# Kernel tuning notes

Hardware: AMD Instinct MI355X
Metric: run time of the kernel (lower is better)

Reference implementation:

```python
import jax, jax.numpy as jnp
import numpy as np

N, E, IN_FEATS, HID, HEADS = 50000, 800000, 256, 32, 8
NEG_SLOPE = 0.2


def _init_params(key):
    ks = jax.random.split(key, 12)
    def lin(k, fi, fo):
        return jax.random.normal(k, (fi, fo), jnp.float32) * (1.0 / np.sqrt(fi))
    p = {}
    # layer 0: in_feats -> HID x HEADS
    p['W0'] = lin(ks[0], IN_FEATS, HEADS * HID)
    p['al0'] = jax.random.normal(ks[1], (HEADS, HID), jnp.float32) * 0.1
    p['ar0'] = jax.random.normal(ks[2], (HEADS, HID), jnp.float32) * 0.1
    p['b0'] = jnp.zeros((HEADS * HID,), jnp.float32)
    # layer 1: HID*HEADS -> HID x HEADS
    p['W1'] = lin(ks[3], HEADS * HID, HEADS * HID)
    p['al1'] = jax.random.normal(ks[4], (HEADS, HID), jnp.float32) * 0.1
    p['ar1'] = jax.random.normal(ks[5], (HEADS, HID), jnp.float32) * 0.1
    p['b1'] = jnp.zeros((HEADS * HID,), jnp.float32)
    # layer 2 (final): HID*HEADS -> HID x 1 head, no activation
    p['W2'] = lin(ks[6], HEADS * HID, HID)
    p['al2'] = jax.random.normal(ks[7], (1, HID), jnp.float32) * 0.1
    p['ar2'] = jax.random.normal(ks[8], (1, HID), jnp.float32) * 0.1
    p['b2'] = jnp.zeros((HID,), jnp.float32)
    return p


def setup_inputs() -> dict:
    key = jax.random.key(0)
    k1, k2, k3, kp = jax.random.split(key, 4)
    inp = {
        'features': jax.random.normal(k1, (N, IN_FEATS), jnp.float32),
        'src': jax.random.randint(k2, (E,), 0, N, jnp.int32),
        'dst': jax.random.randint(k3, (E,), 0, N, jnp.int32),
    }
    inp.update(_init_params(kp))
    return inp


def _gat_layer(x, src, dst, W, al, ar, b, heads, act):
    n = x.shape[0]
    d = W.shape[1] // heads
    feat = (x @ W).reshape(n, heads, d)           # [N,H,D]
    el = jnp.sum(feat * al, axis=-1)              # [N,H]
    er = jnp.sum(feat * ar, axis=-1)              # [N,H]
    e = jax.nn.leaky_relu(el[src] + er[dst], NEG_SLOPE)   # [E,H]
    # segment softmax over destination neighborhoods
    emax = jax.ops.segment_max(e, dst, num_segments=n)
    ex = jnp.exp(e - emax[dst])
    denom = jax.ops.segment_sum(ex, dst, num_segments=n)
    a = ex / (denom[dst] + 1e-9)                  # [E,H]
    msg = feat[src] * a[:, :, None]               # [E,H,D]
    out = jax.ops.segment_sum(msg, dst, num_segments=n)   # [N,H,D]
    out = out + b.reshape(1, heads, d)
    return act(out) if act is not None else out


def reference(features, src, dst, W0, al0, ar0, b0, W1, al1, ar1, b1, W2, al2, ar2, b2):
    h = _gat_layer(features, src, dst, W0, al0, ar0, b0, HEADS, jax.nn.elu)
    h = h.reshape(h.shape[0], -1)
    h = _gat_layer(h, src, dst, W1, al1, ar1, b1, HEADS, jax.nn.elu)
    h = h.reshape(h.shape[0], -1)
    h = _gat_layer(h, src, dst, W2, al2, ar2, b2, 1, None)   # [N,1,D]
    return h.mean(axis=1)                                    # [N,D]
```

## Files before the change

kernel.cpp:

```cpp
#include <hip/hip_runtime.h>

typedef unsigned short u16;
typedef unsigned int   u32;
typedef __attribute__((ext_vector_type(8))) short  short8;
typedef __attribute__((ext_vector_type(4))) float  f32x4;
typedef __attribute__((ext_vector_type(2))) float  f32x2;
typedef __attribute__((ext_vector_type(2))) unsigned int u32v2;
typedef __attribute__((ext_vector_type(4))) unsigned int u32v4;

#define NN 50000
#define NE 800000

__device__ __forceinline__ float bf2f(u16 b) { return __uint_as_float(((u32)b) << 16); }
__device__ __forceinline__ float bflo(u32 p) { return __uint_as_float(p << 16); }
__device__ __forceinline__ float bfhi(u32 p) { return __uint_as_float(p & 0xffff0000u); }
__device__ __forceinline__ u16 f2bf(float f) {
    u32 u = __float_as_uint(f);
    u32 r = u + 0x7fffu + ((u >> 16) & 1u);
    return (u16)(r >> 16);
}
__device__ __forceinline__ float lexp(float v) {
    v = fmaxf(v, 0.2f * v);
    return __expf(fminf(v, 60.f));
}

struct DetectArgs { const u32* p[13]; int nw[13]; };

__global__ __launch_bounds__(256) void k_detect(DetectArgs a, int* flags) {
    __shared__ int sh[256], sz[256];
    int j = blockIdx.x;
    const u32* x = a.p[j];
    int n = a.nw[j];
    int t = threadIdx.x;
    int hits = 0, nz = 0;
    for (int i = t; i < n; i += 256) {
        u32 w = x[i];
        if (w) {
            ++nz;
            u32 e = (w >> 7) & 0xffu;
            if (e >= 100 && e <= 150) ++hits;
        }
    }
    sh[t] = hits; sz[t] = nz;
    __syncthreads();
    for (int ofs = 128; ofs > 0; ofs >>= 1) {
        if (t < ofs) { sh[t] += sh[t + ofs]; sz[t] += sz[t + ofs]; }
        __syncthreads();
    }
    if (t == 0) flags[j] = (sz[0] == 0) ? 2 : ((sh[0] * 2 >= sz[0]) ? 0 : 1);
}

struct ConvArgs { const void* s[9]; float* d[9]; int n[9]; int fi[9]; };

__global__ void k_convert(ConvArgs a, const int* __restrict__ flags) {
    int j = blockIdx.y;
    int i = blockIdx.x * 256 + threadIdx.x;
    if (i >= a.n[j]) return;
    int fl = flags[a.fi[j]];
    float v = 0.f;
    if (fl == 1) v = ((const float*)a.s[j])[i];
    else if (fl == 0) v = bf2f(((const u16*)a.s[j])[i]);
    a.d[j][i] = v;
}

__global__ void k_wpack(const void* __restrict__ Wsrc, const int* __restrict__ flags,
                        int fidx, int N, u16* __restrict__ Wp, int nchunks) {
    int id = blockIdx.x * 256 + threadIdx.x;
    if (id >= nchunks) return;
    int L = id & 63, kt = (id >> 6) & 7, nt = id >> 9;
    int col = nt * 16 + (L & 15);
    int krow = kt * 32 + ((L >> 4) & 3) * 8;
    bool isf32 = (flags[fidx] == 1);
#pragma unroll
    for (int j = 0; j < 8; ++j) {
        int s = (krow + j) * N + col;
        Wp[id * 8 + j] = isf32 ? f2bf(((const float*)Wsrc)[s]) : ((const u16*)Wsrc)[s];
    }
}

__global__ void k_hist(const int* __restrict__ dst, int* __restrict__ deg, int E) {
    int e = blockIdx.x * 256 + threadIdx.x;
    if (e < E) atomicAdd(&deg[dst[e]], 1);
}

__global__ __launch_bounds__(256) void k_scan_partial(const int* __restrict__ deg,
                                                      int* __restrict__ bsum, int n) {
    __shared__ int red[256];
    int t = threadIdx.x;
    int i = blockIdx.x * 256 + t;
    red[t] = (i < n) ? deg[i] : 0;
    __syncthreads();
    for (int ofs = 128; ofs > 0; ofs >>= 1) {
        if (t < ofs) red[t] += red[t + ofs];
        __syncthreads();
    }
    if (t == 0) bsum[blockIdx.x] = red[0];
}

__global__ __launch_bounds__(256) void k_scan_bsum(int* __restrict__ bsum, int nb) {
    __shared__ int s[256];
    int t = threadIdx.x;
    int v = (t < nb) ? bsum[t] : 0;
    s[t] = v;
    __syncthreads();
    for (int ofs = 1; ofs < 256; ofs <<= 1) {
        int x = (t >= ofs) ? s[t - ofs] : 0;
        __syncthreads();
        s[t] += x;
        __syncthreads();
    }
    if (t < nb) bsum[t] = s[t] - v;
}

__global__ __launch_bounds__(256) void k_scan_final(const int* __restrict__ deg,
                                                    const int* __restrict__ bsum,
                                                    int* __restrict__ rowptr,
                                                    int* __restrict__ cursor, int n) {
    __shared__ int s[256];
    int t = threadIdx.x;
    int i = blockIdx.x * 256 + t;
    int v = (i < n) ? deg[i] : 0;
    s[t] = v;
    __syncthreads();
    for (int ofs = 1; ofs < 256; ofs <<= 1) {
        int x = (t >= ofs) ? s[t - ofs] : 0;
        __syncthreads();
        s[t] += x;
        __syncthreads();
    }
    int excl = bsum[blockIdx.x] + s[t] - v;
    if (i < n) {
        rowptr[i] = excl;
        cursor[i] = excl;
        if (i == n - 1) rowptr[n] = excl + v;
    }
}

__global__ void k_scatter(const int* __restrict__ src, const int* __restrict__ dst,
                          int* __restrict__ cursor, int* __restrict__ csr_src, int E) {
    int e = blockIdx.x * 256 + threadIdx.x;
    if (e >= E) return;
    int p = atomicAdd(&cursor[dst[e]], 1);
    csr_src[p] = src[e];
}

__global__ __launch_bounds__(256) void k_gemm_mfma(const void* __restrict__ Xv,
                                                   const int* __restrict__ xflag,
                                                   const u16* __restrict__ Wp,
                                                   u16* __restrict__ OUT, int nrows) {
    __shared__ u16 As[64 * 256];
    const int t = threadIdx.x;
    const int w = t >> 6, L = t & 63;
    const int quad = (L >> 4) & 3;
    const int r0 = blockIdx.x * 64;
    const int nb = blockIdx.y * 8;
    const bool xf32 = (xflag != nullptr) && (*xflag == 1);

    short8* Asv = (short8*)As;
    short8 zero = {0, 0, 0, 0, 0, 0, 0, 0};
#pragma unroll
    for (int i = 0; i < 8; ++i) {
        int g = i * 256 + t;
        int row = g >> 5, cc = g & 31;
        int r = r0 + row;
        short8 val = zero;
        if (r < nrows) {
            if (xf32) {
                const f32x4* Xf4 = (const f32x4*)Xv;
                f32x4 lo = Xf4[(size_t)r * 64 + cc * 2];
                f32x4 hi = Xf4[(size_t)r * 64 + cc * 2 + 1];
                val[0] = (short)f2bf(lo[0]); val[1] = (short)f2bf(lo[1]);
                val[2] = (short)f2bf(lo[2]); val[3] = (short)f2bf(lo[3]);
                val[4] = (short)f2bf(hi[0]); val[5] = (short)f2bf(hi[1]);
                val[6] = (short)f2bf(hi[2]); val[7] = (short)f2bf(hi[3]);
            } else {
                val = ((const short8*)Xv)[(size_t)r * 32 + cc];
            }
        }
        Asv[cc * 64 + (row ^ (cc & 7))] = val;
    }

    const short8* Wv = (const short8*)Wp;
    short8 bf[2][8];
#pragma unroll
    for (int jn = 0; jn < 2; ++jn) {
        int nt = nb + w + jn * 4;
#pragma unroll
        for (int kt = 0; kt < 8; ++kt) bf[jn][kt] = Wv[(nt * 8 + kt) * 64 + L];
    }
    __syncthreads();

    f32x4 acc[4][2];
#pragma unroll
    for (int mi = 0; mi < 4; ++mi)
#pragma unroll
        for (int jn = 0; jn < 2; ++jn) acc[mi][jn] = (f32x4){0.f, 0.f, 0.f, 0.f};

#pragma unroll
    for (int kt = 0; kt < 8; ++kt) {
        const int ccr = kt * 4 + quad;
#pragma unroll
        for (int mi = 0; mi < 4; ++mi) {
            short8 af = Asv[ccr * 64 + ((mi * 16 + (L & 15)) ^ (ccr & 7))];
            acc[mi][0] = __builtin_amdgcn_mfma_f32_16x16x32_bf16(af, bf[0][kt], acc[mi][0], 0, 0, 0);
            acc[mi][1] = __builtin_amdgcn_mfma_f32_16x16x32_bf16(af, bf[1][kt], acc[mi][1], 0, 0, 0);
        }
    }

    const int colbase = blockIdx.y * 128;
#pragma unroll
    for (int mi = 0; mi < 4; ++mi) {
        int rb = r0 + mi * 16 + quad * 4;
#pragma unroll
        for (int jn = 0; jn < 2; ++jn) {
            int c = colbase + (w + jn * 4) * 16 + (L & 15);
            const size_t hb = (size_t)(c >> 5) * nrows * 32 + (c & 31);
#pragma unroll
            for (int reg = 0; reg < 4; ++reg) {
                int r = rb + reg;
                if (r < nrows) OUT[hb + (size_t)r * 32] = f2bf(acc[mi][jn][reg]);
            }
        }
    }
}

__global__ __launch_bounds__(256) void k_gemm_mfma32(const u16* __restrict__ Xb,
                                                     const u16* __restrict__ Wp,
                                                     u16* __restrict__ OUT, int nrows) {
    __shared__ u16 As[128 * 256];
    const int t = threadIdx.x;
    const int w = t >> 6, L = t & 63;
    const int quad = (L >> 4) & 3;
    const int r0 = blockIdx.x * 128;
    const int mh = (w >> 1) * 64, nt = w & 1;

    const short8* Xv = (const short8*)Xb;
    short8* Asv = (short8*)As;
    short8 zero = {0, 0, 0, 0, 0, 0, 0, 0};
#pragma unroll
    for (int i = 0; i < 16; ++i) {
        int g = i * 256 + t;
        int row = g >> 5, cc = g & 31;
        int r = r0 + row;
        Asv[cc * 128 + (row ^ (cc & 7))] = (r < nrows) ? Xv[(size_t)r * 32 + cc] : zero;
    }

    const short8* Wv = (const short8*)Wp;
    short8 bf[8];
#pragma unroll
    for (int kt = 0; kt < 8; ++kt) bf[kt] = Wv[(nt * 8 + kt) * 64 + L];
    __syncthreads();

    f32x4 acc[4];
#pragma unroll
    for (int mi = 0; mi < 4; ++mi) acc[mi] = (f32x4){0.f, 0.f, 0.f, 0.f};

#pragma unroll
    for (int kt = 0; kt < 8; ++kt) {
        const int ccr = kt * 4 + quad;
#pragma unroll
        for (int mi = 0; mi < 4; ++mi) {
            short8 af = Asv[ccr * 128 + ((mh + mi * 16 + (L & 15)) ^ (ccr & 7))];
            acc[mi] = __builtin_amdgcn_mfma_f32_16x16x32_bf16(af, bf[kt], acc[mi], 0, 0, 0);
        }
    }

#pragma unroll
    for (int mi = 0; mi < 4; ++mi) {
        int rb = r0 + mh + mi * 16 + quad * 4;
        int c = nt * 16 + (L & 15);
#pragma unroll
        for (int reg = 0; reg < 4; ++reg) {
            int r = rb + reg;
            if (r < nrows) OUT[(size_t)r * 32 + c] = f2bf(acc[mi][reg]);
        }
    }
}

__global__ void k_elr8(const u16* __restrict__ featT, const float* __restrict__ al,
                       const float* __restrict__ ar, float* __restrict__ elT,
                       float* __restrict__ erT, int n) {
    int node = blockIdx.x * 256 + threadIdx.x;
    int h = blockIdx.y;
    if (node >= n) return;
    const u32v4* fu = (const u32v4*)((const u32*)featT + ((size_t)h * n + node) * 16);
    const float* A = al + h * 32;
    const float* B = ar + h * 32;
    float sl = 0.f, sr = 0.f;
#pragma unroll
    for (int j = 0; j < 4; ++j) {
        u32v4 w4 = fu[j];
#pragma unroll
        for (int k = 0; k < 4; ++k) {
            u32 w = (k == 0) ? w4.x : (k == 1) ? w4.y : (k == 2) ? w4.z : w4.w;
            float f0 = bflo(w), f1 = bfhi(w);
            int c = j * 8 + k * 2;
            sl += f0 * A[c] + f1 * A[c + 1];
            sr += f0 * B[c] + f1 * B[c + 1];
        }
    }
    elT[(size_t)h * n + node] = sl;
    erT[(size_t)h * n + node] = sr;
}

__global__ void k_elr1(const u16* __restrict__ featb, const float* __restrict__ al,
                       const float* __restrict__ ar, float* __restrict__ el,
                       float* __restrict__ er, int n) {
    int node = blockIdx.x * 256 + threadIdx.x;
    if (node >= n) return;
    const u32v4* fu = (const u32v4*)((const u32*)featb + (size_t)node * 16);
    float sl = 0.f, sr = 0.f;
#pragma unroll
    for (int j = 0; j < 4; ++j) {
        u32v4 w4 = fu[j];
#pragma unroll
        for (int k = 0; k < 4; ++k) {
            u32 w = (k == 0) ? w4.x : (k == 1) ? w4.y : (k == 2) ? w4.z : w4.w;
            float f0 = bflo(w), f1 = bfhi(w);
            int c = j * 8 + k * 2;
            sl += f0 * al[c] + f1 * al[c + 1];
            sr += f0 * ar[c] + f1 * ar[c + 1];
        }
    }
    el[node] = sl;
    er[node] = sr;
}

__global__ __launch_bounds__(256) void k_gather8(const int* __restrict__ rowptr,
                                                 const int* __restrict__ csr_src,
                                                 const float* __restrict__ elT,
                                                 const float* __restrict__ erT,
                                                 const u32* __restrict__ featT2,
                                                 const float* __restrict__ bias,
                                                 u32* __restrict__ xout2) {
    const int t = threadIdx.x;
    const int h = blockIdx.x & 7;
    const int g = blockIdx.x >> 3;
    const int d = g * 16 + (t >> 4);
    const int lane = t & 15;
    const int b = rowptr[d], e = rowptr[d + 1];
    const float* __restrict__ elh = elT + (size_t)h * NN;
    const u32* __restrict__ fT = featT2 + (size_t)h * NN * 16;
    const float erd = erT[(size_t)h * NN + d];
    float a0 = 0.f, a1 = 0.f, ssum = 0.f;

    for (int c = b; c < e; c += 16) {
        const int idx = c + lane;
        const int s_own = __builtin_nontemporal_load(csr_src + (idx < e ? idx : e - 1));
        const float ex_own = (idx < e) ? lexp(elh[s_own] + erd) : 0.f;
        ssum += ex_own;
#pragma unroll
        for (int i = 0; i < 16; ++i) {
            const int si = __shfl(s_own, i, 16);
            const float ai = __shfl(ex_own, i, 16);
            const u32 w = fT[(size_t)si * 16 + lane];
            a0 += bflo(w) * ai;
            a1 += bfhi(w) * ai;
        }
    }

    ssum += __shfl_xor(ssum, 1);
    ssum += __shfl_xor(ssum, 2);
    ssum += __shfl_xor(ssum, 4);
    ssum += __shfl_xor(ssum, 8);

    const float rd = 1.f / (ssum + 1e-9f);
    const f32x2 bb = *(const f32x2*)&bias[h * 32 + lane * 2];
    float v0 = a0 * rd + bb[0];
    float v1 = a1 * rd + bb[1];
    v0 = v0 > 0.f ? v0 : expm1f(v0);
    v1 = v1 > 0.f ? v1 : expm1f(v1);
    const u32 o = (u32)f2bf(v0) | ((u32)f2bf(v1) << 16);
    __builtin_nontemporal_store(o, xout2 + ((size_t)d * 128 + h * 16 + lane));
}

__global__ __launch_bounds__(256) void k_gather1(const int* __restrict__ rowptr,
                                                 const int* __restrict__ csr_src,
                                                 const float* __restrict__ el,
                                                 const float* __restrict__ er,
                                                 const u32* __restrict__ featb2,
                                                 const float* __restrict__ bias,
                                                 void* __restrict__ out,
                                                 const int* __restrict__ flag, int n) {
    int t = threadIdx.x;
    int d = blockIdx.x * 16 + (t >> 4);
    int q = t & 15;
    if (d >= n) return;
    int b = rowptr[d], e = rowptr[d + 1];
    float erd = er[d];
    float a0 = 0.f, a1 = 0.f, ssum = 0.f;
    int p = b;
    for (; p + 4 <= e; p += 4) {
        int s0 = csr_src[p], s1 = csr_src[p + 1], s2 = csr_src[p + 2], s3 = csr_src[p + 3];
        float e0 = lexp(el[s0] + erd);
        float e1 = lexp(el[s1] + erd);
        float e2 = lexp(el[s2] + erd);
        float e3 = lexp(el[s3] + erd);
        u32 w0 = featb2[(size_t)s0 * 16 + q];
        u32 w1 = featb2[(size_t)s1 * 16 + q];
        u32 w2 = featb2[(size_t)s2 * 16 + q];
        u32 w3 = featb2[(size_t)s3 * 16 + q];
        a0 += bflo(w0) * e0; a1 += bfhi(w0) * e0;
        a0 += bflo(w1) * e1; a1 += bfhi(w1) * e1;
        a0 += bflo(w2) * e2; a1 += bfhi(w2) * e2;
        a0 += bflo(w3) * e3; a1 += bfhi(w3) * e3;
        ssum += (e0 + e1) + (e2 + e3);
    }
    for (; p < e; ++p) {
        int s = csr_src[p];
        float ev = lexp(el[s] + erd);
        u32 w = featb2[(size_t)s * 16 + q];
        a0 += bflo(w) * ev;
        a1 += bfhi(w) * ev;
        ssum += ev;
    }
    float rd = 1.f / (ssum + 1e-9f);
    float v0 = a0 * rd + bias[2 * q];
    float v1 = a1 * rd + bias[2 * q + 1];
    if (*flag == 1) {
        f32x2 o = {v0, v1};
        ((f32x2*)out)[(size_t)d * 16 + q] = o;
    } else {
        ((u32*)out)[(size_t)d * 16 + q] = (u32)f2bf(v0) | ((u32)f2bf(v1) << 16);
    }
}

extern "C" void kernel_launch(void* const* d_in, const int* in_sizes, int n_in,
                              void* d_out, int out_size, void* d_ws, size_t ws_size,
                              hipStream_t stream) {
    const void* features = d_in[0];
    const int* src = (const int*)d_in[1];
    const int* dst = (const int*)d_in[2];

    char* ws = (char*)d_ws;
    size_t off = 0;
    auto carve = [&](size_t bytes) -> void* {
        void* p = ws + off;
        off = (off + bytes + 255) & ~(size_t)255;
        return p;
    };
    int*   flags = (int*)carve(64);
    float* pconv = (float*)carve(2048 * 4);
    u16*   Wp0 = (u16*)carve(65536 * 2);
    u16*   Wp1 = (u16*)carve(65536 * 2);
    u16*   Wp2 = (u16*)carve(8192 * 2);
    u16*   Xb    = (u16*)carve((size_t)NN * 256 * 2);
    u16*   featb = (u16*)carve((size_t)NN * 256 * 2);
    float* el   = (float*)carve((size_t)NN * 8 * 4);
    float* er   = (float*)carve((size_t)NN * 8 * 4);
    int*   deg     = (int*)carve((size_t)NN * 4);
    int*   cursor  = (int*)carve((size_t)NN * 4);
    int*   rowptr  = (int*)carve((size_t)(NN + 1) * 4);
    int*   bsum    = (int*)carve(256 * 4);
    int*   csr_src = (int*)carve((size_t)NE * 4);
    if (off > ws_size) return;

    const int N = NN, E = NE;
    const int nscan = (N + 255) / 256;

    DetectArgs da;
    const int din_idx[13] = {0, 3, 4, 5, 6, 7, 8, 9, 10, 11, 12, 13, 14};
    for (int j = 0; j < 13; ++j) {
        da.p[j] = (const u32*)d_in[din_idx[j]];
        int nw = in_sizes[din_idx[j]] / 2;
        da.nw[j] = nw > 512 ? 512 : nw;
    }
    k_detect<<<13, 256, 0, stream>>>(da, flags);

    ConvArgs ca;
    const int psl[9] = {4, 5, 6, 8, 9, 10, 12, 13, 14};
    const int pfl[9] = {2, 3, 4, 6, 7, 8, 10, 11, 12};
    float* dsts[9];
    {
        size_t o = 0;
        for (int j = 0; j < 9; ++j) {
            dsts[j] = pconv + o;
            o += (size_t)in_sizes[psl[j]];
        }
    }
    for (int j = 0; j < 9; ++j) {
        ca.s[j] = d_in[psl[j]];
        ca.d[j] = dsts[j];
        ca.n[j] = in_sizes[psl[j]];
        ca.fi[j] = pfl[j];
    }
    k_convert<<<dim3(1, 9), 256, 0, stream>>>(ca, flags);
    float* al0f = dsts[0]; float* ar0f = dsts[1]; float* b0f = dsts[2];
    float* al1f = dsts[3]; float* ar1f = dsts[4]; float* b1f = dsts[5];
    float* al2f = dsts[6]; float* ar2f = dsts[7]; float* b2f = dsts[8];

    k_wpack<<<32, 256, 0, stream>>>(d_in[3],  flags, 1, 256, Wp0, 8192);
    k_wpack<<<32, 256, 0, stream>>>(d_in[7],  flags, 5, 256, Wp1, 8192);
    k_wpack<<<4,  256, 0, stream>>>(d_in[11], flags, 9, 32,  Wp2, 1024);

    hipMemsetAsync(deg, 0, (size_t)N * 4, stream);
    k_hist<<<(E + 255) / 256, 256, 0, stream>>>(dst, deg, E);
    k_scan_partial<<<nscan, 256, 0, stream>>>(deg, bsum, N);
    k_scan_bsum<<<1, 256, 0, stream>>>(bsum, nscan);
    k_scan_final<<<nscan, 256, 0, stream>>>(deg, bsum, rowptr, cursor, N);
    k_scatter<<<(E + 255) / 256, 256, 0, stream>>>(src, dst, cursor, csr_src, E);

    const dim3 ggrid((N + 63) / 64, 2);
    const dim3 egrid(nscan, 8);
    const int ggrid8 = 8 * (N / 16);

    k_gemm_mfma<<<ggrid, 256, 0, stream>>>(features, flags, Wp0, featb, N);
    k_elr8<<<egrid, 256, 0, stream>>>(featb, al0f, ar0f, el, er, N);
    k_gather8<<<ggrid8, 256, 0, stream>>>(rowptr, csr_src, el, er,
                                          (const u32*)featb, b0f, (u32*)Xb);

    k_gemm_mfma<<<ggrid, 256, 0, stream>>>(Xb, nullptr, Wp1, featb, N);
    k_elr8<<<egrid, 256, 0, stream>>>(featb, al1f, ar1f, el, er, N);
    k_gather8<<<ggrid8, 256, 0, stream>>>(rowptr, csr_src, el, er,
                                          (const u32*)featb, b1f, (u32*)Xb);

    k_gemm_mfma32<<<(N + 127) / 128, 256, 0, stream>>>(Xb, Wp2, featb, N);
    k_elr1<<<(N + 255) / 256, 256, 0, stream>>>(featb, al2f, ar2f, el, er, N);
    k_gather1<<<(N + 15) / 16, 256, 0, stream>>>(rowptr, csr_src, el, er,
                                                 (const u32*)featb, b2f,
                                                 d_out, flags, N);
}
```

Baseline: 490.1 us.

## Map one wavefront per destination node in per-head gather with LDS edge staging

The per-head gather kernel now assigns a full 64-lane wavefront to each destination node instead of 16 lanes. Each lane loads 8 bytes, and 8 edges are processed in parallel per iteration. Source indices and exp weights are staged through shared memory rather than broadcast by shuffles. Partial sums are reduced across lane groups at the end. The aim is more memory-level parallelism and wider loads on irregular neighbor rows, at the cost of four times as many blocks, extra cross-lane reductions, and idle lanes for low-degree nodes.

```diff
diff --git a/kernel.cpp b/kernel.cpp
--- a/kernel.cpp
+++ b/kernel.cpp
@@ -333,45 +333,68 @@
                                                  const u32* __restrict__ featT2,
                                                  const float* __restrict__ bias,
                                                  u32* __restrict__ xout2) {
+    __shared__ u32v2 sbuf[4][64];
     const int t = threadIdx.x;
+    const int wv = t >> 6;
+    const int lane = t & 63;
     const int h = blockIdx.x & 7;
-    const int g = blockIdx.x >> 3;
-    const int d = g * 16 + (t >> 4);
-    const int lane = t & 15;
+    const int d = (blockIdx.x >> 3) * 4 + wv;
+    const int j8 = lane >> 3, c8 = lane & 7;
     const int b = rowptr[d], e = rowptr[d + 1];
+    const int deg = e - b;
     const float* __restrict__ elh = elT + (size_t)h * NN;
-    const u32* __restrict__ fT = featT2 + (size_t)h * NN * 16;
+    const u32v2* __restrict__ fv = (const u32v2*)(featT2 + (size_t)h * NN * 16);
     const float erd = erT[(size_t)h * NN + d];
-    float a0 = 0.f, a1 = 0.f, ssum = 0.f;
-
-    for (int c = b; c < e; c += 16) {
-        const int idx = c + lane;
-        const int s_own = __builtin_nontemporal_load(csr_src + (idx < e ? idx : e - 1));
-        const float ex_own = (idx < e) ? lexp(elh[s_own] + erd) : 0.f;
+    u32v2* __restrict__ sb = sbuf[wv];
+
+    float a0 = 0.f, a1 = 0.f, a2 = 0.f, a3 = 0.f, ssum = 0.f;
+
+    for (int c = 0; c < deg; c += 64) {
+        const int nv = deg - c < 64 ? deg - c : 64;
+        const int idx = b + c + (lane < nv ? lane : nv - 1);
+        const int s_own = __builtin_nontemporal_load(csr_src + idx);
+        const float ex_own = (lane < nv) ? lexp(elh[s_own] + erd) : 0.f;
         ssum += ex_own;
-#pragma unroll
-        for (int i = 0; i < 16; ++i) {
-            const int si = __shfl(s_own, i, 16);
-            const float ai = __shfl(ex_own, i, 16);
-            const u32 w = fT[(size_t)si * 16 + lane];
-            a0 += bflo(w) * ai;
-            a1 += bfhi(w) * ai;
-        }
-    }
-
-    ssum += __shfl_xor(ssum, 1);
-    ssum += __shfl_xor(ssum, 2);
-    ssum += __shfl_xor(ssum, 4);
-    ssum += __shfl_xor(ssum, 8);
-
-    const float rd = 1.f / (ssum + 1e-9f);
-    const f32x2 bb = *(const f32x2*)&bias[h * 32 + lane * 2];
-    float v0 = a0 * rd + bb[0];
-    float v1 = a1 * rd + bb[1];
-    v0 = v0 > 0.f ? v0 : expm1f(v0);
-    v1 = v1 > 0.f ? v1 : expm1f(v1);
-    const u32 o = (u32)f2bf(v0) | ((u32)f2bf(v1) << 16);
-    __builtin_nontemporal_store(o, xout2 + ((size_t)d * 128 + h * 16 + lane));
+        u32v2 pr;
+        pr.x = (u32)s_own;
+        pr.y = __float_as_uint(ex_own);
+        sb[lane] = pr;
+        __builtin_amdgcn_sched_barrier(0);
+        const int ni = (nv + 7) >> 3;
+        for (int i = 0; i < ni; ++i) {
+            const u32v2 pr2 = sb[i * 8 + j8];
+            const float ai = __uint_as_float(pr2.y);
+            const u32v2 w = fv[(size_t)pr2.x * 8 + c8];
+            a0 += bflo(w.x) * ai; a1 += bfhi(w.x) * ai;
+            a2 += bflo(w.y) * ai; a3 += bfhi(w.y) * ai;
+        }
+        __builtin_amdgcn_sched_barrier(0);
+    }
+
+    a0 += __shfl_xor(a0, 8); a0 += __shfl_xor(a0, 16); a0 += __shfl_xor(a0, 32);
+    a1 += __shfl_xor(a1, 8); a1 += __shfl_xor(a1, 16); a1 += __shfl_xor(a1, 32);
+    a2 += __shfl_xor(a2, 8); a2 += __shfl_xor(a2, 16); a2 += __shfl_xor(a2, 32);
+    a3 += __shfl_xor(a3, 8); a3 += __shfl_xor(a3, 16); a3 += __shfl_xor(a3, 32);
+    ssum += __shfl_xor(ssum, 1);  ssum += __shfl_xor(ssum, 2);
+    ssum += __shfl_xor(ssum, 4);  ssum += __shfl_xor(ssum, 8);
+    ssum += __shfl_xor(ssum, 16); ssum += __shfl_xor(ssum, 32);
+
+    if (j8 == 0) {
+        const float rd = 1.f / (ssum + 1e-9f);
+        const f32x4 bb = *(const f32x4*)&bias[h * 32 + c8 * 4];
+        float v0 = a0 * rd + bb[0];
+        float v1 = a1 * rd + bb[1];
+        float v2 = a2 * rd + bb[2];
+        float v3 = a3 * rd + bb[3];
+        v0 = v0 > 0.f ? v0 : expm1f(v0);
+        v1 = v1 > 0.f ? v1 : expm1f(v1);
+        v2 = v2 > 0.f ? v2 : expm1f(v2);
+        v3 = v3 > 0.f ? v3 : expm1f(v3);
+        u32v2 o;
+        o.x = (u32)f2bf(v0) | ((u32)f2bf(v1) << 16);
+        o.y = (u32)f2bf(v2) | ((u32)f2bf(v3) << 16);
+        __builtin_nontemporal_store(o, (u32v2*)xout2 + ((size_t)d * 64 + h * 8 + c8));
+    }
 }
 
 __global__ __launch_bounds__(256) void k_gather1(const int* __restrict__ rowptr,
@@ -502,7 +525,7 @@
 
     const dim3 ggrid((N + 63) / 64, 2);
     const dim3 egrid(nscan, 8);
-    const int ggrid8 = 8 * (N / 16);
+    const int ggrid8 = 8 * (N / 4);
 
     k_gemm_mfma<<<ggrid, 256, 0, stream>>>(features, flags, Wp0, featb, N);
     k_elr8<<<egrid, 256, 0, stream>>>(featb, al0f, ar0f, el, er, N);
```

New measurement: 661.8 us. 1.35x slower.
